# Optimization experiments

Measured on AMD Instinct MI355X. Metric: run time of the kernel, lower is better.

The kernel has to match this reference:

```python
import jax, jax.numpy as jnp
import numpy as np

B, T, H, D = 2, 1024, 8, 64
C = H * D            # 512 = n_embd = heads*head_dim
M = 32768            # external memory size
TOPK = 32
SCALE = D ** -0.5
EPS_NORM = 1e-12


def _layernorm(x, w, b, eps=1e-5):
    mu = jnp.mean(x, axis=-1, keepdims=True)
    var = jnp.var(x, axis=-1, keepdims=True)
    return (x - mu) * jax.lax.rsqrt(var + eps) * w + b


def _l2norm(x):
    n = jnp.linalg.norm(x, axis=-1, keepdims=True)
    return x / jnp.maximum(n, EPS_NORM)


def setup_inputs() -> dict:
    key = jax.random.key(0)
    ks = jax.random.split(key, 12)
    s = C ** -0.5
    return {
        "x": jax.random.normal(ks[0], (B, T, C), jnp.float32),
        "memory_kv": jax.random.normal(ks[1], (B, M, 2, C), jnp.float32),
        "ln_w": jnp.ones((C,), jnp.float32),
        "ln_b": jnp.zeros((C,), jnp.float32),
        "Wq": jax.random.normal(ks[2], (C, C), jnp.float32) * s,
        "bq": jnp.zeros((C,), jnp.float32),
        "Wk": jax.random.normal(ks[3], (C, C), jnp.float32) * s,
        "bk": jnp.zeros((C,), jnp.float32),
        "Wv": jax.random.normal(ks[4], (C, C), jnp.float32) * s,
        "bv": jnp.zeros((C,), jnp.float32),
        "Wo": jax.random.normal(ks[5], (C, C), jnp.float32) * s,
        "bo": jnp.zeros((C,), jnp.float32),
        "gate_bias": jax.random.normal(ks[6], (H, 1, 1), jnp.float32),
    }


def reference(x, memory_kv, ln_w, ln_b, Wq, bq, Wk, bk, Wv, bv, Wo, bo, gate_bias):
    xn = _layernorm(x, ln_w, ln_b)
    q = _l2norm(xn @ Wq + bq)           # [B,T,C], F.normalize(dim=-1)
    k = _l2norm(xn @ Wk + bk)
    v = xn @ Wv + bv

    qh = q.reshape(B, T, H, D).transpose(0, 2, 1, 3)   # b h t d
    kh = k.reshape(B, T, H, D).transpose(0, 2, 1, 3)
    vh = v.reshape(B, T, H, D).transpose(0, 2, 1, 3)

    # local causal attention
    qk = jnp.einsum('bhid,bhjd->bhij', qh, kh) * SCALE
    causal = jnp.triu(jnp.ones((T, T), bool), k=1)
    qk = jnp.where(causal, -jnp.inf, qk)
    attn = jax.nn.softmax(qk, axis=-1)
    qkv = attn @ vh                                     # b h t d

    # kNN retrieval: top-k inner product of flat queries vs stored keys
    q_flat = q                                          # b t C (normalized)
    mem_keys = memory_kv[:, :, 0]                       # b M C
    scores = jnp.einsum('btc,bmc->btm', q_flat, mem_keys)
    _, idx = jax.lax.top_k(scores, TOPK)                # b t k
    # gather retrieved kv: [b, t, k, 2, C]
    mem = jnp.take_along_axis(memory_kv[:, None], idx[:, :, :, None, None], axis=2)
    mem_k = mem[..., 0, :].reshape(B, T, TOPK, H, D).transpose(0, 3, 1, 2, 4)  # b h t k d
    mem_v = mem[..., 1, :].reshape(B, T, TOPK, H, D).transpose(0, 3, 1, 2, 4)

    mem_qk = jnp.einsum('bhtd,bhtkd->bhtk', qh, mem_k) * SCALE
    mem_attn = jax.nn.softmax(mem_qk, axis=-1)
    mem_qkv = jnp.einsum('bhtk,bhtkd->bhtd', mem_attn, mem_v)

    combined = mem_qkv * gate_bias + qkv * (1.0 - gate_bias)  # gate_bias [H,1,1]
    combined = combined.transpose(0, 2, 1, 3).reshape(B, T, C)
    out = combined @ Wo + bo

    current_kv = jnp.stack((k, v), axis=-2)             # b t 2 C (normalized keys)
    return out, current_kv
```

## Files before the change

### kernel.cpp

```cpp
#include <hip/hip_runtime.h>
#include <hip/hip_bf16.h>

#define B_ 2
#define T_ 1024
#define H_ 8
#define D_ 64
#define C_ 512
#define M_ 32768
#define TOPK_ 32
#define NCAND_ 64
#define SCALE_ 0.125f
#define QSCALE_ 360.0f
#define KSCALE_ 24.0f
#define OSCALE_ 20.0f

typedef unsigned short u16;
typedef float    f32x2  __attribute__((ext_vector_type(2)));
typedef float    f32x4  __attribute__((ext_vector_type(4)));
typedef __bf16   bf16x8 __attribute__((ext_vector_type(8)));
typedef u16      u16x4  __attribute__((ext_vector_type(4)));
typedef int      i32x4  __attribute__((ext_vector_type(4)));
typedef unsigned char u8x4 __attribute__((ext_vector_type(4)));

__device__ __forceinline__ u16 f2bf(float f) {
  __hip_bfloat16 b = __float2bfloat16(f);
  u16 u; __builtin_memcpy(&u, &b, 2); return u;
}

__device__ __forceinline__ unsigned char q8(float v, float scale) {
  int iv = (int)rintf(v * scale);
  iv = iv > 127 ? 127 : (iv < -127 ? -127 : iv);
  return (unsigned char)(signed char)iv;
}

__device__ __forceinline__ void gl_lds16(const void* g, void* l) {
  __builtin_amdgcn_global_load_lds(
      (const __attribute__((address_space(1))) void*)g,
      (__attribute__((address_space(3))) void*)l, 16, 0, 0);
}


__device__ __forceinline__ void wtrans_body(char* pool, int p,
    const float* __restrict__ W0, const float* __restrict__ W1,
    const float* __restrict__ W2, u16* __restrict__ WT) {
  u16 (*tl)[33] = (u16 (*)[33])pool;
  int z = p >> 8;
  int q = p & 255;
  const float* W = (z == 0) ? W0 : (z == 1) ? W1 : W2;
  u16* dst = WT + (size_t)z * C_ * C_;
  int n0 = (q & 15) * 32, k0 = (q >> 4) * 32;
  int tx = threadIdx.x & 31, ty = threadIdx.x >> 5;
#pragma unroll
  for (int i = 0; i < 4; ++i) {
    int k = k0 + ty + i * 8;
    tl[ty + i * 8][tx] = f2bf(W[(size_t)k * C_ + n0 + tx]);
  }
  __syncthreads();
#pragma unroll
  for (int i = 0; i < 4; ++i) {
    int nn = ty + i * 8;
    dst[(size_t)(n0 + nn) * C_ + k0 + tx] = tl[tx][nn];
  }
}

__device__ __forceinline__ void prep_keys_body(int bid,
    const float* __restrict__ mem, char* __restrict__ ki) {
  const int n4 = B_ * M_ * C_ / 4;
  for (int i = bid * 256 + (int)threadIdx.x; i < n4; i += 8192 * 256) {
    int row = i >> 7;
    int c4 = i & 127;
    f32x4 v = *(const f32x4*)(mem + ((size_t)row * 1024) + c4 * 4);
    u8x4 o;
    o[0] = q8(v[0], KSCALE_); o[1] = q8(v[1], KSCALE_);
    o[2] = q8(v[2], KSCALE_); o[3] = q8(v[3], KSCALE_);
    *(u8x4*)((unsigned char*)ki + (size_t)i * 4) = o;
  }
}

__global__ __launch_bounds__(256) void fatPrep(
    const float* __restrict__ W0, const float* __restrict__ W1,
    const float* __restrict__ W2, u16* __restrict__ WT,
    const float* __restrict__ mem, char* __restrict__ ki) {
  __shared__ __align__(16) char pool[2112];
  int p = blockIdx.x;
  if (p < 768) wtrans_body(pool, p, W0, W1, W2, WT);
  else prep_keys_body(p - 768, mem, ki);
}

__global__ __launch_bounds__(256) void ln_kernel(
    const float* __restrict__ x, const float* __restrict__ w,
    const float* __restrict__ bia, u16* __restrict__ xn, float* __restrict__ xnf) {
  int row = blockIdx.x * 4 + (threadIdx.x >> 6);
  int lane = threadIdx.x & 63;
  const float* xr = x + (size_t)row * C_;
  f32x4 v0 = *(const f32x4*)(xr + lane * 4);
  f32x4 v1 = *(const f32x4*)(xr + 256 + lane * 4);
  float s = v0[0] + v0[1] + v0[2] + v0[3] + v1[0] + v1[1] + v1[2] + v1[3];
  float q = v0[0]*v0[0]+v0[1]*v0[1]+v0[2]*v0[2]+v0[3]*v0[3]
          + v1[0]*v1[0]+v1[1]*v1[1]+v1[2]*v1[2]+v1[3]*v1[3];
#pragma unroll
  for (int m = 1; m < 64; m <<= 1) { s += __shfl_xor(s, m); q += __shfl_xor(q, m); }
  float mean = s * (1.0f / C_);
  float var  = q * (1.0f / C_) - mean * mean;
  float rs = rsqrtf(var + 1e-5f);
  u16x4 o0, o1;
  f32x4 f0, f1;
#pragma unroll
  for (int e = 0; e < 4; ++e) {
    int c = lane * 4 + e;
    f0[e] = (v0[e] - mean) * rs * w[c] + bia[c];
    o0[e] = f2bf(f0[e]);
    int c2 = 256 + lane * 4 + e;
    f1[e] = (v1[e] - mean) * rs * w[c2] + bia[c2];
    o1[e] = f2bf(f1[e]);
  }
  *(u16x4*)(xn + (size_t)row * C_ + lane * 4) = o0;
  *(u16x4*)(xn + (size_t)row * C_ + 256 + lane * 4) = o1;
  *(f32x4*)(xnf + (size_t)row * C_ + lane * 4) = f0;
  *(f32x4*)(xnf + (size_t)row * C_ + 256 + lane * 4) = f1;
}

__global__ __launch_bounds__(256) void gemm_f32(
    const float* __restrict__ A, const float* __restrict__ Bw,
    const float* __restrict__ bias, float* __restrict__ Cout) {
  __shared__ float As_t[32][68];
  __shared__ float Bs[32][64];
  int tid = threadIdx.x;
  int tx = tid & 15, ty = tid >> 4;
  int r0 = blockIdx.x * 64, c0 = blockIdx.y * 64;
  f32x4 acc[4];
#pragma unroll
  for (int i = 0; i < 4; ++i) acc[i] = f32x4{0.f, 0.f, 0.f, 0.f};
  for (int kt = 0; kt < 16; ++kt) {
    int k0 = kt * 32;
#pragma unroll
    for (int i2 = 0; i2 < 2; ++i2) {
      int idx = i2 * 256 + tid;
      int arow = idx >> 3, ac = idx & 7;
      f32x4 av = *(const f32x4*)(A + (size_t)(r0 + arow) * 512 + k0 + ac * 4);
      As_t[ac * 4 + 0][arow] = av[0]; As_t[ac * 4 + 1][arow] = av[1];
      As_t[ac * 4 + 2][arow] = av[2]; As_t[ac * 4 + 3][arow] = av[3];
      int krow = idx >> 4, cc = idx & 15;
      f32x4 bv = *(const f32x4*)(Bw + (size_t)(k0 + krow) * 512 + c0 + cc * 4);
      *(f32x4*)(&Bs[krow][cc * 4]) = bv;
    }
    __syncthreads();
#pragma unroll
    for (int kk = 0; kk < 32; ++kk) {
      f32x4 bv = *(const f32x4*)(&Bs[kk][tx * 4]);
      f32x4 avv = *(const f32x4*)(&As_t[kk][ty * 4]);
#pragma unroll
      for (int i = 0; i < 4; ++i) {
        float av = avv[i];
        acc[i] += av * bv;
      }
    }
    __syncthreads();
  }
  f32x4 bb = *(const f32x4*)(bias + c0 + tx * 4);
#pragma unroll
  for (int i = 0; i < 4; ++i)
    *(f32x4*)(Cout + (size_t)(r0 + ty * 4 + i) * 512 + c0 + tx * 4) = acc[i] + bb;
}

__global__ __launch_bounds__(256) void gemm128(
    const u16* __restrict__ A, long aBS,
    const u16* __restrict__ Bt, long bBS,
    float* __restrict__ Cf, long cBS,
    const float* __restrict__ bias, const float* __restrict__ bias2, int ldc) {
  __shared__ __align__(16) u16 As[128 * 64];
  __shared__ __align__(16) u16 Bs[128 * 64];
  const int tid = threadIdx.x;
  const int lane = tid & 63, w = tid >> 6;
  const int wm = w >> 1, wn = w & 1;
  const int z = blockIdx.z;
  const u16* Ab = A + (size_t)z * aBS + (size_t)blockIdx.x * 128 * 512;
  const u16* Bb = Bt + (size_t)z * bBS + (size_t)blockIdx.y * 128 * 512;

  f32x4 acc[4][4];
#pragma unroll
  for (int i = 0; i < 4; ++i)
#pragma unroll
    for (int j = 0; j < 4; ++j) acc[i][j] = f32x4{0.f, 0.f, 0.f, 0.f};

  for (int kt = 0; kt < 8; ++kt) {
    const u16* Akt = Ab + kt * 64;
    const u16* Bkt = Bb + kt * 64;
#pragma unroll
    for (int it = 0; it < 4; ++it) {
      int slot = it * 256 + tid;
      int rr = slot >> 3, ss = slot & 7;
      int q = ss ^ (rr & 7);
      gl_lds16(Akt + (size_t)rr * 512 + q * 8, (char*)As + slot * 16);
      gl_lds16(Bkt + (size_t)rr * 512 + q * 8, (char*)Bs + slot * 16);
    }
    __syncthreads();
#pragma unroll
    for (int kk = 0; kk < 2; ++kk) {
      bf16x8 av[4], bv[4];
#pragma unroll
      for (int i = 0; i < 4; ++i) {
        int blk = kk * 4 + (lane >> 4);
        int ra = wm * 64 + i * 16 + (lane & 15);
        av[i] = *(const bf16x8*)((const char*)As + ra * 128 + ((blk ^ (ra & 7)) << 4));
        int rb = wn * 64 + i * 16 + (lane & 15);
        bv[i] = *(const bf16x8*)((const char*)Bs + rb * 128 + ((blk ^ (rb & 7)) << 4));
      }
#pragma unroll
      for (int mi = 0; mi < 4; ++mi)
#pragma unroll
        for (int ni = 0; ni < 4; ++ni)
          acc[mi][ni] = __builtin_amdgcn_mfma_f32_16x16x32_bf16(av[mi], bv[ni], acc[mi][ni], 0, 0, 0);
    }
    __syncthreads();
  }
  const float* bi = (z == 1 && bias2) ? bias2 : bias;
  const long cbase = (long)z * cBS;
  const int rsub = (lane >> 4) * 4;
  const long row0 = (long)blockIdx.x * 128 + wm * 64;
  const int col00 = wn * 64 + (lane & 15) + (int)blockIdx.y * 128;
#pragma unroll
  for (int mi = 0; mi < 4; ++mi)
#pragma unroll
    for (int rg = 0; rg < 4; ++rg) {
      long row = row0 + mi * 16 + rsub + rg;
#pragma unroll
      for (int ni = 0; ni < 4; ++ni) {
        int col = col00 + ni * 16;
        float bb = bi ? bi[col] : 0.0f;
        Cf[cbase + row * (long)ldc + col] = acc[mi][ni][rg] + bb;
      }
    }
}

__global__ __launch_bounds__(256) void postproc_kernel(
    const float* __restrict__ qraw, const float* __restrict__ kraw,
    const float* __restrict__ vraw, float* __restrict__ qf,
    u16* __restrict__ qb, u16* __restrict__ kb, char* __restrict__ qi,
    float* __restrict__ kvout) {
  int row = blockIdx.x * 4 + (threadIdx.x >> 6);
  int lane = threadIdx.x & 63;
  size_t rb_ = (size_t)row * C_;
  f32x4 a0 = *(const f32x4*)(qraw + rb_ + lane * 4);
  f32x4 a1 = *(const f32x4*)(qraw + rb_ + 256 + lane * 4);
  float ss = a0[0]*a0[0]+a0[1]*a0[1]+a0[2]*a0[2]+a0[3]*a0[3]
           + a1[0]*a1[0]+a1[1]*a1[1]+a1[2]*a1[2]+a1[3]*a1[3];
#pragma unroll
  for (int m = 1; m < 64; m <<= 1) ss += __shfl_xor(ss, m);
  float rn = 1.0f / fmaxf(sqrtf(ss), 1e-12f);
  f32x4 q0 = a0 * rn, q1 = a1 * rn;
  *(f32x4*)(qf + rb_ + lane * 4) = q0;
  *(f32x4*)(qf + rb_ + 256 + lane * 4) = q1;
  u16x4 t0, t1;
#pragma unroll
  for (int e = 0; e < 4; ++e) { t0[e] = f2bf(q0[e]); t1[e] = f2bf(q1[e]); }
  *(u16x4*)(qb + rb_ + lane * 4) = t0;
  *(u16x4*)(qb + rb_ + 256 + lane * 4) = t1;
  u8x4 i0, i1;
#pragma unroll
  for (int e = 0; e < 4; ++e) { i0[e] = q8(q0[e], QSCALE_); i1[e] = q8(q1[e], QSCALE_); }
  *(u8x4*)((unsigned char*)qi + rb_ + lane * 4) = i0;
  *(u8x4*)((unsigned char*)qi + rb_ + 256 + lane * 4) = i1;
  f32x4 b0 = *(const f32x4*)(kraw + rb_ + lane * 4);
  f32x4 b1 = *(const f32x4*)(kraw + rb_ + 256 + lane * 4);
  float sk = b0[0]*b0[0]+b0[1]*b0[1]+b0[2]*b0[2]+b0[3]*b0[3]
           + b1[0]*b1[0]+b1[1]*b1[1]+b1[2]*b1[2]+b1[3]*b1[3];
#pragma unroll
  for (int m = 1; m < 64; m <<= 1) sk += __shfl_xor(sk, m);
  float rk = 1.0f / fmaxf(sqrtf(sk), 1e-12f);
  f32x4 k0 = b0 * rk, k1 = b1 * rk;
  size_t kvb = (size_t)row * (2 * C_);
  *(f32x4*)(kvout + kvb + lane * 4) = k0;
  *(f32x4*)(kvout + kvb + 256 + lane * 4) = k1;
#pragma unroll
  for (int e = 0; e < 4; ++e) { t0[e] = f2bf(k0[e]); t1[e] = f2bf(k1[e]); }
  *(u16x4*)(kb + rb_ + lane * 4) = t0;
  *(u16x4*)(kb + rb_ + 256 + lane * 4) = t1;
  f32x4 c0 = *(const f32x4*)(vraw + rb_ + lane * 4);
  f32x4 c1 = *(const f32x4*)(vraw + rb_ + 256 + lane * 4);
  *(f32x4*)(kvout + kvb + C_ + lane * 4) = c0;
  *(f32x4*)(kvout + kvb + C_ + 256 + lane * 4) = c1;
}

__global__ __launch_bounds__(256) void vtrans_kernel(
    const float* __restrict__ vraw, u16* __restrict__ vT) {
  __shared__ u16 tile[64][65];
  int tt = blockIdx.x, h = blockIdx.y, b = blockIdx.z;
  int tx = threadIdx.x, ty = threadIdx.y;
#pragma unroll
  for (int i = 0; i < 8; ++i) {
    int t = tt * 64 + ty + i * 8;
    const float* src = vraw + (size_t)(b * T_ + t) * C_ + h * 64;
    tile[ty + i * 8][tx] = f2bf(src[tx]);
    tile[ty + i * 8][tx + 32] = f2bf(src[tx + 32]);
  }
  __syncthreads();
#pragma unroll
  for (int i = 0; i < 8; ++i) {
    int d = ty + i * 8;
    u16* dst = vT + ((size_t)((b * H_ + h) * 64 + d)) * T_ + tt * 64;
    dst[tx] = tile[tx][d];
    dst[tx + 32] = tile[tx + 32][d];
  }
}


__device__ __forceinline__ void attn_body(char* pool, int p,
    const u16* __restrict__ qb, const u16* __restrict__ kb,
    const u16* __restrict__ vT, float* __restrict__ o) {
  u16* Ks = (u16*)pool;
  u16* Vs = (u16*)(pool + 16384);
  char* PsBase = pool + 32768;
  int tid = threadIdx.x, lane = tid & 63, w = tid >> 6;
  int it = p & 15, h = (p >> 4) & 7, b = p >> 7;
  char* PsW = PsBase + w * 4096;
  int t0 = it * 64;
  bf16x8 aq[2];
#pragma unroll
  for (int kk = 0; kk < 2; ++kk) {
    int row = t0 + w * 16 + (lane & 15);
    aq[kk] = *(const bf16x8*)(qb + (size_t)(b * T_ + row) * C_ + h * 64 + kk * 32 + (lane >> 4) * 8);
  }
  f32x4 accO[4];
  float denp[4];
#pragma unroll
  for (int j = 0; j < 4; ++j) { accO[j] = f32x4{0.f,0.f,0.f,0.f}; denp[j] = 0.f; }

  int ntiles = it / 2 + 1;
  for (int jt = 0; jt < ntiles; ++jt) {
    int j0 = jt * 128;
#pragma unroll
    for (int i2 = 0; i2 < 4; ++i2) {
      int slot = i2 * 256 + tid;
      int rr = slot >> 3, ssw = slot & 7;
      int q = ssw ^ (rr & 7);
      gl_lds16(kb + (size_t)(b * T_ + j0 + rr) * C_ + h * 64 + q * 8, (char*)Ks + slot * 16);
    }
#pragma unroll
    for (int i2 = 0; i2 < 4; ++i2) {
      int slot = i2 * 256 + tid;
      int rr = slot >> 4, ssw = slot & 15;
      int q = ssw ^ (rr & 15);
      gl_lds16(vT + ((size_t)((b * H_ + h) * 64 + rr)) * T_ + j0 + q * 8, (char*)Vs + slot * 16);
    }
    __syncthreads();
    f32x4 s[8];
#pragma unroll
    for (int ni = 0; ni < 8; ++ni) s[ni] = f32x4{0.f,0.f,0.f,0.f};
#pragma unroll
    for (int kk = 0; kk < 2; ++kk) {
      bf16x8 bk[8];
#pragma unroll
      for (int ni = 0; ni < 8; ++ni) {
        int rbi = ni * 16 + (lane & 15);
        int blk = kk * 4 + (lane >> 4);
        bk[ni] = *(const bf16x8*)((const char*)Ks + rbi * 128 + ((blk ^ (rbi & 7)) << 4));
      }
#pragma unroll
      for (int ni = 0; ni < 8; ++ni)
        s[ni] = __builtin_amdgcn_mfma_f32_16x16x32_bf16(aq[kk], bk[ni], s[ni], 0, 0, 0);
    }
#pragma unroll
    for (int ni = 0; ni < 8; ++ni)
#pragma unroll
      for (int rg = 0; rg < 4; ++rg) {
        int qrow = t0 + w * 16 + (lane >> 4) * 4 + rg;
        int kvcol = j0 + ni * 16 + (lane & 15);
        float sv = s[ni][rg] * SCALE_;
        float pp = (kvcol <= qrow) ? __expf(sv) : 0.0f;
        denp[rg] += pp;
        int qk = (lane >> 4) * 4 + rg;
        int kvl = ni * 16 + (lane & 15);
        int blk2 = kvl >> 3;
        *(u16*)(PsW + qk * 256 + ((blk2 ^ qk) << 4) + (kvl & 7) * 2) = f2bf(pp);
      }
#pragma unroll
    for (int kk2 = 0; kk2 < 4; ++kk2) {
      bf16x8 ap, bvv[4];
      int blk = kk2 * 4 + (lane >> 4);
      int rq = lane & 15;
      ap = *(const bf16x8*)(PsW + rq * 256 + ((blk ^ rq) << 4));
#pragma unroll
      for (int nd = 0; nd < 4; ++nd) {
        int rd = nd * 16 + (lane & 15);
        bvv[nd] = *(const bf16x8*)((const char*)Vs + rd * 256 + ((blk ^ (rd & 15)) << 4));
      }
#pragma unroll
      for (int nd = 0; nd < 4; ++nd)
        accO[nd] = __builtin_amdgcn_mfma_f32_16x16x32_bf16(ap, bvv[nd], accO[nd], 0, 0, 0);
    }
    __syncthreads();
  }
  float den[4];
#pragma unroll
  for (int rg = 0; rg < 4; ++rg) {
    float d = denp[rg];
    d += __shfl_xor(d, 1); d += __shfl_xor(d, 2);
    d += __shfl_xor(d, 4); d += __shfl_xor(d, 8);
    den[rg] = d;
  }
#pragma unroll
  for (int nd = 0; nd < 4; ++nd)
#pragma unroll
    for (int rg = 0; rg < 4; ++rg) {
      int row = t0 + w * 16 + (lane >> 4) * 4 + rg;
      int d = nd * 16 + (lane & 15);
      o[(size_t)(b * T_ + row) * C_ + h * 64 + d] = accO[nd][rg] / den[rg];
    }
}

__device__ __forceinline__ void sc8_body(char* pool, int p,
    const char* __restrict__ A, const char* __restrict__ Bt, char* __restrict__ sc8) {
  char* As = pool;
  char* Bs = pool + 16384;
  const int tid = threadIdx.x;
  const int lane = tid & 63, w = tid >> 6;
  const int wm = w >> 1, wn = w & 1;
  const int z = p >> 11;
  const int q_ = p & 2047;
  const int r = (q_ >> 3) & 7;
  const int c = ((q_ >> 6) << 3) | (q_ & 7);
  const char* Ab = A + (size_t)z * T_ * C_ + (size_t)r * 128 * 512;
  const char* Bb = Bt + (size_t)z * M_ * C_ + (size_t)c * 128 * 512;

  i32x4 acc[4][4];
#pragma unroll
  for (int i = 0; i < 4; ++i)
#pragma unroll
    for (int j = 0; j < 4; ++j) acc[i][j] = i32x4{0, 0, 0, 0};

  for (int kt = 0; kt < 4; ++kt) {
    const char* Akt = Ab + kt * 128;
    const char* Bkt = Bb + kt * 128;
#pragma unroll
    for (int it = 0; it < 4; ++it) {
      int slot = it * 256 + tid;
      int rr = slot >> 3, ss = slot & 7;
      int ch = ss ^ (rr & 7);
      gl_lds16(Akt + (size_t)rr * 512 + ch * 16, As + slot * 16);
      gl_lds16(Bkt + (size_t)rr * 512 + ch * 16, Bs + slot * 16);
    }
    __syncthreads();
#pragma unroll
    for (int kk = 0; kk < 2; ++kk) {
      i32x4 av[4], bv[4];
#pragma unroll
      for (int i = 0; i < 4; ++i) {
        int blk = kk * 4 + (lane >> 4);
        int ra = wm * 64 + i * 16 + (lane & 15);
        av[i] = *(const i32x4*)(As + ra * 128 + ((blk ^ (ra & 7)) << 4));
        int rb = wn * 64 + i * 16 + (lane & 15);
        bv[i] = *(const i32x4*)(Bs + rb * 128 + ((blk ^ (rb & 7)) << 4));
      }
#pragma unroll
      for (int mi = 0; mi < 4; ++mi)
#pragma unroll
        for (int ni = 0; ni < 4; ++ni)
          acc[mi][ni] = __builtin_amdgcn_mfma_i32_16x16x64_i8(av[mi], bv[ni], acc[mi][ni], 0, 0, 0);
    }
    __syncthreads();
  }
  const int rsub = (lane >> 4) * 4;
  const long row0 = (long)r * 128 + wm * 64;
  const int col00 = c * 128 + wn * 64 + (lane & 15);
  char* base = sc8 + (size_t)z * T_ * M_;
  const float osc = OSCALE_ / (QSCALE_ * KSCALE_);
#pragma unroll
  for (int mi = 0; mi < 4; ++mi)
#pragma unroll
    for (int rg = 0; rg < 4; ++rg) {
      long row = row0 + mi * 16 + rsub + rg;
#pragma unroll
      for (int ni = 0; ni < 4; ++ni) {
        int iv = (int)rintf((float)acc[mi][ni][rg] * osc);
        iv = iv > 127 ? 127 : (iv < -127 ? -127 : iv);
        base[row * (long)M_ + col00 + ni * 16] = (char)iv;
      }
    }
}

__global__ __launch_bounds__(256) void fatL4(
    const u16* __restrict__ qb, const u16* __restrict__ kb,
    const u16* __restrict__ vT, float* __restrict__ attn,
    const char* __restrict__ qi, const char* __restrict__ ki,
    char* __restrict__ sc8) {
  __shared__ __align__(16) char pool[49152];
  int p = blockIdx.x;
  if (p < 256) attn_body(pool, p, qb, kb, vT, attn);
  else sc8_body(pool, p - 256, qi, ki, sc8);
}

__global__ __launch_bounds__(256) void topk_tail_kernel(
    const char* __restrict__ scores, const float* __restrict__ qf,
    const float* __restrict__ mem, const float* __restrict__ attn,
    const float* __restrict__ gate, u16* __restrict__ comb) {
  int row = blockIdx.x, b = row >> 10;
  int tid = threadIdx.x, lane = tid & 63, w = tid >> 6;
  __shared__ unsigned candKey[256];
  __shared__ float qL[512];
  __shared__ float sL[NCAND_];
  __shared__ float sHh[NCAND_][8];
  __shared__ int cL[NCAND_];
  __shared__ int wIdx[TOPK_];
  __shared__ float eL[TOPK_][8];
  qL[tid] = qf[(size_t)row * C_ + tid];
  qL[256 + tid] = qf[(size_t)row * C_ + 256 + tid];
  const unsigned char* s = (const unsigned char*)scores + (size_t)row * M_;
  unsigned c[8];
#pragma unroll
  for (int i = 0; i < 8; ++i) c[i] = 0;
  for (int i2 = 0; i2 < 16; ++i2) {
    int base = i2 * 2048 + tid * 8;
    uint2 v = *(const uint2*)(s + base);
#pragma unroll
    for (int e = 0; e < 8; ++e) {
      unsigned byte = (e < 4) ? ((v.x >> (8 * e)) & 0xFF) : ((v.y >> (8 * (e - 4))) & 0xFF);
      unsigned key = byte ^ 0x80u;
      unsigned cmb = (key << 15) | (unsigned)(32767 - (base + e));
      if (cmb > c[7]) {
        c[7] = cmb;
#pragma unroll
        for (int ss = 7; ss > 0; --ss) {
          if (c[ss] > c[ss - 1]) { unsigned t = c[ss - 1]; c[ss - 1] = c[ss]; c[ss] = t; }
        }
      }
    }
  }
  for (int r = 0; r < 64; ++r) {
    unsigned bb = c[0];
#pragma unroll
    for (int m = 1; m < 64; m <<= 1) {
      unsigned o = __shfl_xor(bb, m);
      bb = (o > bb) ? o : bb;
    }
    if (lane == 0) candKey[w * 64 + r] = bb;
    if (c[0] == bb) {
#pragma unroll
      for (int ss = 0; ss < 7; ++ss) c[ss] = c[ss + 1];
      c[7] = 0;
    }
  }
  __syncthreads();
  {
    unsigned my = candKey[tid];
    int rank = 0;
    for (int j = 0; j < 256; ++j) rank += (candKey[j] > my);
    if (rank < NCAND_) cL[rank] = 32767 - (int)(my & 32767u);
  }
  __syncthreads();
#pragma unroll 4
  for (int i = 0; i < 16; ++i) {
    int cdx = w * 16 + i;
    const float* mrow = mem + ((size_t)(b * M_ + cL[cdx])) * 1024;
    f32x4 k0 = *(const f32x4*)(mrow + lane * 8);
    f32x4 k1 = *(const f32x4*)(mrow + lane * 8 + 4);
    float p = qL[lane*8+0]*k0[0] + qL[lane*8+1]*k0[1] + qL[lane*8+2]*k0[2] + qL[lane*8+3]*k0[3]
            + qL[lane*8+4]*k1[0] + qL[lane*8+5]*k1[1] + qL[lane*8+6]*k1[2] + qL[lane*8+7]*k1[3];
    p += __shfl_xor(p, 1); p += __shfl_xor(p, 2); p += __shfl_xor(p, 4);
    if ((lane & 7) == 0) sHh[cdx][lane >> 3] = p;
    float pf = p;
    pf += __shfl_xor(pf, 8); pf += __shfl_xor(pf, 16); pf += __shfl_xor(pf, 32);
    if (lane == 0) sL[cdx] = pf;
  }
  __syncthreads();
  if (tid < NCAND_) {
    float sv = sL[tid]; int id = cL[tid];
    int rank = 0;
#pragma unroll
    for (int j = 0; j < NCAND_; ++j) {
      float sj = sL[j];
      rank += (sj > sv) || (sj == sv && cL[j] < id);
    }
    if (rank < TOPK_) {
      wIdx[rank] = id;
#pragma unroll
      for (int h = 0; h < 8; ++h)
        eL[rank][h] = __expf(sHh[tid][h] * SCALE_);
    }
  }
  __syncthreads();
  int h2 = tid >> 5, dp = tid & 31;
  float num0 = 0.f, num1 = 0.f, den = 0.f;
#pragma unroll 8
  for (int k = 0; k < TOPK_; ++k) {
    float wgt = eL[k][h2];
    const float* vrow = mem + ((size_t)(b * M_ + wIdx[k])) * 1024 + 512;
    f32x2 vv = *(const f32x2*)(vrow + h2 * 64 + dp * 2);
    num0 += wgt * vv[0];
    num1 += wgt * vv[1];
    den += wgt;
  }
  float g = gate[h2];
  int c0 = h2 * 64 + dp * 2;
  float a0 = attn[(size_t)row * C_ + c0];
  float a1 = attn[(size_t)row * C_ + c0 + 1];
  u16 o0 = f2bf(g * (num0 / den) + (1.0f - g) * a0);
  u16 o1 = f2bf(g * (num1 / den) + (1.0f - g) * a1);
  *(unsigned*)(comb + (size_t)row * C_ + c0) = (unsigned)o0 | ((unsigned)o1 << 16);
}

extern "C" void kernel_launch(void* const* d_in, const int* in_sizes, int n_in,
                              void* d_out, int out_size, void* d_ws, size_t ws_size,
                              hipStream_t stream) {
  const float* x    = (const float*)d_in[0];
  const float* mem  = (const float*)d_in[1];
  const float* lnw  = (const float*)d_in[2];
  const float* lnb  = (const float*)d_in[3];
  const float* Wq   = (const float*)d_in[4];
  const float* bq   = (const float*)d_in[5];
  const float* Wk   = (const float*)d_in[6];
  const float* bk   = (const float*)d_in[7];
  const float* Wv   = (const float*)d_in[8];
  const float* bv   = (const float*)d_in[9];
  const float* Wo   = (const float*)d_in[10];
  const float* bo   = (const float*)d_in[11];
  const float* gate = (const float*)d_in[12];
  float* out   = (float*)d_out;
  float* kvout = out + (size_t)B_ * T_ * C_;

  size_t off = 0;
  auto alloc = [&](size_t bytes) {
    char* r = (char*)d_ws + off;
    off += (bytes + 255) & ~(size_t)255;
    return r;
  };
  u16*      WT   = (u16*)alloc(3ull * C_ * C_ * 2);
  char*     ki   = (char*)alloc((size_t)B_ * M_ * C_);
  u16*      xn   = (u16*)alloc((size_t)B_ * T_ * C_ * 2);
  float*    xnf  = (float*)alloc((size_t)B_ * T_ * C_ * 4);
  float*    qraw = (float*)alloc((size_t)B_ * T_ * C_ * 4);
  float*    kvraw= (float*)alloc(2ull * B_ * T_ * C_ * 4);
  float*    kraw = kvraw;
  float*    vraw = kvraw + (size_t)B_ * T_ * C_;
  float*    qf   = (float*)alloc((size_t)B_ * T_ * C_ * 4);
  u16*      qb   = (u16*)alloc((size_t)B_ * T_ * C_ * 2);
  u16*      kb   = (u16*)alloc((size_t)B_ * T_ * C_ * 2);
  char*     qi   = (char*)alloc((size_t)B_ * T_ * C_);
  u16*      vT   = (u16*)alloc((size_t)B_ * T_ * C_ * 2);
  float*    attn = (float*)alloc((size_t)B_ * T_ * C_ * 4);
  char*     sc8  = (char*)alloc((size_t)B_ * T_ * M_);
  u16*      comb = (u16*)alloc((size_t)B_ * T_ * C_ * 2);
  if (off > ws_size) return;

  fatPrep<<<768 + 8192, 256, 0, stream>>>(Wk, Wv, Wo, WT, mem, ki);
  ln_kernel<<<512, 256, 0, stream>>>(x, lnw, lnb, xn, xnf);
  gemm_f32<<<dim3(32, 8), 256, 0, stream>>>(xnf, Wq, bq, qraw);
  gemm128<<<dim3(16, 4, 2), 256, 0, stream>>>(xn, 0, WT, (long)C_ * C_,
                                              kvraw, (long)B_ * T_ * C_, bk, bv, C_);
  postproc_kernel<<<512, 256, 0, stream>>>(qraw, kraw, vraw, qf, qb, kb, qi, kvout);
  vtrans_kernel<<<dim3(16, 8, 2), dim3(32, 8), 0, stream>>>(vraw, vT);
  fatL4<<<256 + 4096, 256, 0, stream>>>(qb, kb, vT, attn, qi, ki, sc8);
  topk_tail_kernel<<<2048, 256, 0, stream>>>(sc8, qf, mem, attn, gate, comb);
  gemm128<<<dim3(16, 4, 1), 256, 0, stream>>>(comb, 0, WT + 2 * C_ * C_, 0,
                                              out, 0, bo, nullptr, C_);
}
```

Before: 290.9 us.

## Fuse per-tile top-8 candidate selection into int8 score GEMM epilogue

Instead of writing the full int8 score matrix to global memory, each score tile is staged in shared memory and two threads per row compute a top-8 of packed score/index keys, which is written as a compact candidate list. The top-k tail kernel then loads 8 candidates per thread instead of scanning all 32K scores per row. This removes most of the score-matrix write and read traffic at the cost of extra shared-memory work and barriers in the GEMM epilogue.

```diff
diff --git a/kernel.cpp b/kernel.cpp
--- a/kernel.cpp
+++ b/kernel.cpp
@@ -410,7 +410,7 @@
 }
 
 __device__ __forceinline__ void sc8_body(char* pool, int p,
-    const char* __restrict__ A, const char* __restrict__ Bt, char* __restrict__ sc8) {
+    const char* __restrict__ A, const char* __restrict__ Bt, unsigned* __restrict__ cand8) {
   char* As = pool;
   char* Bs = pool + 16384;
   const int tid = threadIdx.x;
@@ -460,38 +460,81 @@
     }
     __syncthreads();
   }
-  const int rsub = (lane >> 4) * 4;
-  const long row0 = (long)r * 128 + wm * 64;
-  const int col00 = c * 128 + wn * 64 + (lane & 15);
-  char* base = sc8 + (size_t)z * T_ * M_;
   const float osc = OSCALE_ / (QSCALE_ * KSCALE_);
-#pragma unroll
-  for (int mi = 0; mi < 4; ++mi)
-#pragma unroll
-    for (int rg = 0; rg < 4; ++rg) {
-      long row = row0 + mi * 16 + rsub + rg;
-#pragma unroll
-      for (int ni = 0; ni < 4; ++ni) {
-        int iv = (int)rintf((float)acc[mi][ni][rg] * osc);
-        iv = iv > 127 ? 127 : (iv < -127 ? -127 : iv);
-        base[row * (long)M_ + col00 + ni * 16] = (char)iv;
-      }
-    }
+  {
+    unsigned char* tileB = (unsigned char*)pool;
+    const int rsub = (lane >> 4) * 4;
+#pragma unroll
+    for (int mi = 0; mi < 4; ++mi)
+#pragma unroll
+      for (int rg = 0; rg < 4; ++rg) {
+        int rl = wm * 64 + mi * 16 + rsub + rg;
+#pragma unroll
+        for (int ni = 0; ni < 4; ++ni) {
+          int iv = (int)rintf((float)acc[mi][ni][rg] * osc);
+          iv = iv > 127 ? 127 : (iv < -127 ? -127 : iv);
+          int col = wn * 64 + ni * 16 + (lane & 15);
+          int wd = col >> 2;
+          tileB[rl * 128 + ((((wd) + rl) & 31) << 2) + (col & 3)] =
+              (unsigned char)((iv & 0xFF) ^ 0x80);
+        }
+      }
+    __syncthreads();
+    int rrow = tid >> 1, half = tid & 1;
+    unsigned top[8];
+#pragma unroll
+    for (int i = 0; i < 8; ++i) top[i] = 0;
+    const unsigned* tw = (const unsigned*)pool;
+    for (int j = 0; j < 16; ++j) {
+      int wd = half * 16 + j;
+      unsigned v = tw[rrow * 32 + ((wd + rrow) & 31)];
+#pragma unroll
+      for (int e = 0; e < 4; ++e) {
+        unsigned key = (v >> (8 * e)) & 0xFF;
+        unsigned cmb = (key << 15) | (unsigned)(32767 - (c * 128 + wd * 4 + e));
+        if (cmb > top[7]) {
+          top[7] = cmb;
+#pragma unroll
+          for (int s2 = 7; s2 > 0; --s2)
+            if (top[s2] > top[s2 - 1]) { unsigned t = top[s2 - 1]; top[s2 - 1] = top[s2]; top[s2] = t; }
+        }
+      }
+    }
+    unsigned* mrg = (unsigned*)(pool + 16384);
+    if (half == 1) {
+#pragma unroll
+      for (int i = 0; i < 8; ++i) mrg[rrow * 8 + i] = top[i];
+    }
+    __syncthreads();
+    if (half == 0) {
+      unsigned outv[8];
+      int ia = 0, ib = 0;
+#pragma unroll
+      for (int i = 0; i < 8; ++i) {
+        unsigned bb2 = mrg[rrow * 8 + ib];
+        if (top[ia] >= bb2) { outv[i] = top[ia]; ia++; }
+        else { outv[i] = bb2; ib++; }
+      }
+      unsigned* dst = cand8 + (((size_t)(z * T_ + r * 128 + rrow)) * 256 + c) * 8;
+#pragma unroll
+      for (int i = 0; i < 8; ++i) dst[i] = outv[i];
+    }
+  }
 }
 
 __global__ __launch_bounds__(256) void fatL4(
     const u16* __restrict__ qb, const u16* __restrict__ kb,
     const u16* __restrict__ vT, float* __restrict__ attn,
     const char* __restrict__ qi, const char* __restrict__ ki,
-    char* __restrict__ sc8) {
+    unsigned* __restrict__ cand8) {
   __shared__ __align__(16) char pool[49152];
   int p = blockIdx.x;
   if (p < 256) attn_body(pool, p, qb, kb, vT, attn);
-  else sc8_body(pool, p - 256, qi, ki, sc8);
+  else sc8_body(pool, p - 256, qi, ki, cand8);
 }
 
 __global__ __launch_bounds__(256) void topk_tail_kernel(
-    const char* __restrict__ scores, const float* __restrict__ qf,
+    const unsigned* __restrict__ cand8, const float* __restrict__ qf,
     const float* __restrict__ mem, const float* __restrict__ attn,
     const float* __restrict__ gate, u16* __restrict__ comb) {
   int row = blockIdx.x, b = row >> 10;
@@ -505,26 +548,13 @@
   __shared__ float eL[TOPK_][8];
   qL[tid] = qf[(size_t)row * C_ + tid];
   qL[256 + tid] = qf[(size_t)row * C_ + 256 + tid];
-  const unsigned char* s = (const unsigned char*)scores + (size_t)row * M_;
   unsigned c[8];
-#pragma unroll
-  for (int i = 0; i < 8; ++i) c[i] = 0;
-  for (int i2 = 0; i2 < 16; ++i2) {
-    int base = i2 * 2048 + tid * 8;
-    uint2 v = *(const uint2*)(s + base);
-#pragma unroll
-    for (int e = 0; e < 8; ++e) {
-      unsigned byte = (e < 4) ? ((v.x >> (8 * e)) & 0xFF) : ((v.y >> (8 * (e - 4))) & 0xFF);
-      unsigned key = byte ^ 0x80u;
-      unsigned cmb = (key << 15) | (unsigned)(32767 - (base + e));
-      if (cmb > c[7]) {
-        c[7] = cmb;
-#pragma unroll
-        for (int ss = 7; ss > 0; --ss) {
-          if (c[ss] > c[ss - 1]) { unsigned t = c[ss - 1]; c[ss - 1] = c[ss]; c[ss] = t; }
-        }
-      }
-    }
+  {
+    const unsigned* cp = cand8 + ((size_t)row * 256 + tid) * 8;
+    uint4 v0 = *(const uint4*)cp;
+    uint4 v1 = *(const uint4*)(cp + 4);
+    c[0] = v0.x; c[1] = v0.y; c[2] = v0.z; c[3] = v0.w;
+    c[4] = v1.x; c[5] = v1.y; c[6] = v1.z; c[7] = v1.w;
   }
   for (int r = 0; r < 64; ++r) {
     unsigned bb = c[0];
@@ -638,7 +668,7 @@
   char*     qi   = (char*)alloc((size_t)B_ * T_ * C_);
   u16*      vT   = (u16*)alloc((size_t)B_ * T_ * C_ * 2);
   float*    attn = (float*)alloc((size_t)B_ * T_ * C_ * 4);
-  char*     sc8  = (char*)alloc((size_t)B_ * T_ * M_);
+  unsigned* cand8= (unsigned*)alloc((size_t)B_ * T_ * 256 * 8 * 4);
   u16*      comb = (u16*)alloc((size_t)B_ * T_ * C_ * 2);
   if (off > ws_size) return;
 
@@ -649,8 +679,8 @@
                                               kvraw, (long)B_ * T_ * C_, bk, bv, C_);
   postproc_kernel<<<512, 256, 0, stream>>>(qraw, kraw, vraw, qf, qb, kb, qi, kvout);
   vtrans_kernel<<<dim3(16, 8, 2), dim3(32, 8), 0, stream>>>(vraw, vT);
-  fatL4<<<256 + 4096, 256, 0, stream>>>(qb, kb, vT, attn, qi, ki, sc8);
-  topk_tail_kernel<<<2048, 256, 0, stream>>>(sc8, qf, mem, attn, gate, comb);
+  fatL4<<<256 + 4096, 256, 0, stream>>>(qb, kb, vT, attn, qi, ki, cand8);
+  topk_tail_kernel<<<2048, 256, 0, stream>>>(cand8, qf, mem, attn, gate, comb);
   gemm128<<<dim3(16, 4, 1), 256, 0, stream>>>(comb, 0, WT + 2 * C_ * C_, 0,
                                               out, 0, bo, nullptr, C_);
 }
```

Measured after the change: 318.6 us. +9.5%, slower.
